# Kernel optimization log

Hardware: AMD Instinct MI355X
Metric: run time of the kernel (lower is better)

Reference implementation:

```python
import jax, jax.numpy as jnp
import numpy as np

B, S, E = 2, 2048, 1024
INNER = 2048          # proj_factor * embedding_dim
NH = 4                # mLSTM heads
K = 4                 # causal conv kernel size
PH, PD = 512, 4       # headwise-proj heads (inner/qkv_proj_blocksize) and block size


def setup_inputs() -> dict:
    key = jax.random.key(0)
    ks = jax.random.split(key, 10)
    f = lambda k, shape, s=0.02: jax.random.normal(k, shape, jnp.float32) * s
    return dict(
        x=jax.random.normal(ks[0], (B, S, E), jnp.float32),
        W_up=f(ks[1], (E, 2 * INNER)),
        conv_w=f(ks[2], (K, INNER), 0.1),
        conv_b=jnp.zeros((INNER,), jnp.float32),
        Wq=f(ks[3], (PH, PD, PD), 0.3),
        Wk=f(ks[4], (PH, PD, PD), 0.3),
        Wv=f(ks[5], (PH, PD, PD), 0.3),
        W_ig=f(ks[6], (3 * INNER, NH), 0.01),
        b_ig=jnp.zeros((NH,), jnp.float32),
        W_fg=f(ks[7], (3 * INNER, NH), 0.01),
        b_fg=jnp.linspace(3.0, 6.0, NH).astype(jnp.float32),
        norm_w=jnp.ones((INNER,), jnp.float32),
        skip=jnp.ones((INNER,), jnp.float32),
        W_down=f(ks[8], (INNER, E)),
    )


def _forward(x, W_up, conv_w, conv_b, Wq, Wk, Wv, W_ig, b_ig, W_fg, b_fg,
             norm_w, skip, W_down):
    Bx, Sx, _ = x.shape
    # up projection then split into mlstm branch and gate branch z
    x_inner = x @ W_up                                  # (B,S,2*INNER)
    x_mlstm, z = jnp.split(x_inner, 2, axis=-1)
    # causal depthwise conv1d (left-pad K-1)
    Kk = conv_w.shape[0]
    x_pad = jnp.pad(x_mlstm, ((0, 0), (Kk - 1, 0), (0, 0)))
    x_conv = sum(x_pad[:, i:i + Sx, :] * conv_w[i] for i in range(Kk)) + conv_b
    x_act = jax.nn.swish(x_conv)

    def headwise(t, W):
        H, o, d = W.shape
        return jnp.einsum('bshd,hod->bsho', t.reshape(Bx, Sx, H, d), W).reshape(Bx, Sx, H * o)

    q = headwise(x_act, Wq)
    k = headwise(x_act, Wk)
    v = headwise(x_mlstm, Wv)
    Dm = q.shape[-1]
    NHn = b_ig.shape[0]
    DH = Dm // NHn
    qh = q.reshape(Bx, Sx, NHn, DH).transpose(0, 2, 1, 3)   # (B,NH,S,DH)
    kh = k.reshape(Bx, Sx, NHn, DH).transpose(0, 2, 1, 3)
    vh = v.reshape(Bx, Sx, NHn, DH).transpose(0, 2, 1, 3)
    # input / forget gate preactivations from concat(q,k,v)
    if_in = jnp.concatenate([q, k, v], axis=-1)             # (B,S,3*INNER)
    ig = (if_in @ W_ig + b_ig).transpose(0, 2, 1)[..., None]  # (B,NH,S,1)
    fg = (if_in @ W_fg + b_fg).transpose(0, 2, 1)[..., None]
    # parallel stabilized mLSTM (matrix memory, exp gating)
    log_f = jax.nn.log_sigmoid(fg)
    lfc = jnp.concatenate([jnp.zeros((Bx, NHn, 1, 1), log_f.dtype),
                           jnp.cumsum(log_f, axis=2)], axis=2)  # (B,NH,S+1,1)
    lfm = lfc - jnp.swapaxes(lfc, -2, -1)                   # (B,NH,S+1,S+1)
    mask = jnp.tril(jnp.ones((Sx + 1, Sx + 1), bool))
    lfm = jnp.where(mask, lfm, -jnp.inf)[:, :, 1:, 1:]      # (B,NH,S,S)
    logD = lfm + jnp.swapaxes(ig, -2, -1)
    mD = jnp.max(logD, axis=-1, keepdims=True)
    Dmat = jnp.exp(logD - mD)
    C = jnp.einsum('bnsd,bntd->bnst', qh, kh) * (DH ** -0.5) * Dmat
    norm = jnp.maximum(jnp.abs(C.sum(-1, keepdims=True)), jnp.exp(-mD))
    h = jnp.einsum('bnst,bntd->bnsd', C / (norm + 1e-6), vh)  # (B,NH,S,DH)
    # multi-head layernorm over DH, then merge heads
    mu = h.mean(-1, keepdims=True)
    var = ((h - mu) ** 2).mean(-1, keepdims=True)
    hn = ((h - mu) * jax.lax.rsqrt(var + 1e-6)).transpose(0, 2, 1, 3).reshape(Bx, Sx, Dm)
    hn = hn * norm_w
    # learnable skip from conv activation, gate with swish(z), down proj
    h_state = (hn + skip * x_act) * jax.nn.swish(z)
    return h_state @ W_down


def reference(x, W_up, conv_w, conv_b, Wq, Wk, Wv, W_ig, b_ig, W_fg, b_fg,
              norm_w, skip, W_down):
    return _forward(x, W_up, conv_w, conv_b, Wq, Wk, Wv, W_ig, b_ig, W_fg,
                    b_fg, norm_w, skip, W_down)
```

## Files before the change

kernel.cpp:

```cpp
#include <hip/hip_runtime.h>
#include <math.h>

#define S_LEN 2048
#define INNERD 2048
#define NHEAD 4
#define DHEAD 512
#define BATCH 2
#define SCALE_QK 0.044194173824159216f

typedef __attribute__((ext_vector_type(8))) short short8v;
typedef __attribute__((ext_vector_type(4))) float f32x4;

#define MFMA_BF16(A, B, C) __builtin_amdgcn_mfma_f32_16x16x32_bf16(A, B, C, 0, 0, 0)

__device__ __forceinline__ void gll16(const void* g, void* l) {
  __builtin_amdgcn_global_load_lds((const __attribute__((address_space(1))) unsigned int*)g,
                                   (__attribute__((address_space(3))) unsigned int*)l,
                                   16, 0, 0);
}

__device__ __forceinline__ unsigned short f2bf(float x) {
  union { float f; unsigned u; } v; v.f = x;
  unsigned r = v.u + 0x7FFFu + ((v.u >> 16) & 1u);
  return (unsigned short)(r >> 16);
}
__device__ __forceinline__ float bf2f(unsigned short x) {
  union { unsigned u; float f; } v; v.u = ((unsigned)x) << 16; return v.f;
}
__device__ __forceinline__ float swishf(float x) { return x / (1.0f + __expf(-x)); }
__device__ __forceinline__ float logsigf(float x) {
  return (x >= 0.0f) ? -log1pf(expf(-x)) : (x - log1pf(expf(x)));
}

__global__ __launch_bounds__(256) void cast_kernel(const float* __restrict__ src,
                                                   unsigned short* __restrict__ dst) {
  const int i = (blockIdx.x * 256 + threadIdx.x) * 8;
  const float4 a = *(const float4*)(src + i);
  const float4 b = *(const float4*)(src + i + 4);
  short8v o;
  o[0] = (short)f2bf(a.x); o[1] = (short)f2bf(a.y); o[2] = (short)f2bf(a.z); o[3] = (short)f2bf(a.w);
  o[4] = (short)f2bf(b.x); o[5] = (short)f2bf(b.y); o[6] = (short)f2bf(b.z); o[7] = (short)f2bf(b.w);
  *(short8v*)(dst + i) = o;
}

__global__ __launch_bounds__(256) void trc_kernel(const float* __restrict__ src,
                                                  unsigned short* __restrict__ dst,
                                                  int R, int C) {
  const int t = threadIdx.x;
  const int r0 = blockIdx.y * 128, c0 = blockIdx.x * 128;
  const int rb = (t >> 4) * 8, cb2 = (t & 15) * 8;
  float vreg[8][8];
#pragma unroll
  for (int u = 0; u < 8; ++u) {
    const float4 p0 = *(const float4*)(src + (size_t)(r0 + rb + u) * C + c0 + cb2);
    const float4 p1 = *(const float4*)(src + (size_t)(r0 + rb + u) * C + c0 + cb2 + 4);
    vreg[u][0] = p0.x; vreg[u][1] = p0.y; vreg[u][2] = p0.z; vreg[u][3] = p0.w;
    vreg[u][4] = p1.x; vreg[u][5] = p1.y; vreg[u][6] = p1.z; vreg[u][7] = p1.w;
  }
#pragma unroll
  for (int j = 0; j < 8; ++j) {
    short8v o;
#pragma unroll
    for (int u = 0; u < 8; ++u) o[u] = (short)f2bf(vreg[u][j]);
    *(short8v*)(dst + (size_t)(c0 + cb2 + j) * R + r0 + rb) = o;
  }
}

__global__ __launch_bounds__(256) void trv_kernel(const unsigned short* __restrict__ v,
                                                  unsigned short* __restrict__ vt) {
  const int t = threadIdx.x;
  const int s0 = blockIdx.x * 128;
  const int d0 = blockIdx.y * 128;
  const int bn = blockIdx.z;
  const int b = bn >> 2, n = bn & 3;
  const int sb = (t >> 4) * 8, db = (t & 15) * 8;
  unsigned short r[8][8];
#pragma unroll
  for (int u = 0; u < 8; ++u) {
    const short8v x2 = *(const short8v*)(v + (size_t)(b * S_LEN + s0 + sb + u) * INNERD + n * DHEAD + d0 + db);
#pragma unroll
    for (int j = 0; j < 8; ++j) r[u][j] = (unsigned short)x2[j];
  }
#pragma unroll
  for (int j = 0; j < 8; ++j) {
    short8v o;
#pragma unroll
    for (int u = 0; u < 8; ++u) o[u] = (short)r[u][j];
    *(short8v*)(vt + (size_t)(bn * DHEAD + d0 + db + j) * S_LEN + s0 + sb) = o;
  }
}

__global__ __launch_bounds__(256) void prep_kernel(
    const float* __restrict__ Wq, const float* __restrict__ Wk, const float* __restrict__ Wv,
    const float* __restrict__ Wig, const float* __restrict__ Wfg,
    unsigned short* __restrict__ Wpk, unsigned short* __restrict__ CgT) {
  const int t = threadIdx.x;
  float wq[2][16], wk[2][16], wv[2][16];
#pragma unroll
  for (int hh = 0; hh < 2; ++hh) {
    const int h = 2 * t + hh;
#pragma unroll
    for (int j = 0; j < 16; ++j) {
      wq[hh][j] = Wq[(size_t)h * 16 + j];
      wk[hh][j] = Wk[(size_t)h * 16 + j];
      wv[hh][j] = Wv[(size_t)h * 16 + j];
    }
  }
#pragma unroll
  for (int hh = 0; hh < 2; ++hh)
#pragma unroll
    for (int sub = 0; sub < 2; ++sub) {
      short8v oq, ok, ov;
#pragma unroll
      for (int j = 0; j < 8; ++j) {
        oq[j] = (short)f2bf(wq[hh][sub * 8 + j]);
        ok[j] = (short)f2bf(wk[hh][sub * 8 + j]);
        ov[j] = (short)f2bf(wv[hh][sub * 8 + j]);
      }
      *(short8v*)(Wpk + ((size_t)(0 + hh * 2 + sub) * 256 + t) * 8) = oq;
      *(short8v*)(Wpk + ((size_t)(4 + hh * 2 + sub) * 256 + t) * 8) = ok;
      *(short8v*)(Wpk + ((size_t)(8 + hh * 2 + sub) * 256 + t) * 8) = ov;
    }
#pragma unroll
  for (int u = 0; u < 8; ++u) {
    const int hh = u >> 2, d = u & 3;
    const int h = 2 * t + hh;
    float cia[4] = {0, 0, 0, 0}, cim[4] = {0, 0, 0, 0};
    float cfa[4] = {0, 0, 0, 0}, cfm[4] = {0, 0, 0, 0};
#pragma unroll
    for (int o = 0; o < 4; ++o) {
      const int row = h * 4 + o;
      const float aq = wq[hh][o * 4 + d], ak = wk[hh][o * 4 + d], av = wv[hh][o * 4 + d];
#pragma unroll
      for (int g = 0; g < 4; ++g) {
        cia[g] += aq * Wig[(size_t)row * 4 + g] + ak * Wig[(size_t)(INNERD + row) * 4 + g];
        cim[g] += av * Wig[(size_t)(2 * INNERD + row) * 4 + g];
        cfa[g] += aq * Wfg[(size_t)row * 4 + g] + ak * Wfg[(size_t)(INNERD + row) * 4 + g];
        cfm[g] += av * Wfg[(size_t)(2 * INNERD + row) * 4 + g];
      }
    }
    const int c = t * 8 + u;
#pragma unroll
    for (int g = 0; g < 4; ++g) {
      CgT[(size_t)(g) * INNERD + c] = f2bf(cia[g]);
      CgT[(size_t)(4 + g) * INNERD + c] = f2bf(cim[g]);
      CgT[(size_t)(8 + g) * INNERD + c] = f2bf(cfa[g]);
      CgT[(size_t)(12 + g) * INNERD + c] = f2bf(cfm[g]);
    }
  }
}

template <int OUTMODE>
__global__ __launch_bounds__(256) void gemm_bf16(const unsigned short* __restrict__ A,
                                                 const unsigned short* __restrict__ Bt,
                                                 float* __restrict__ Cf,
                                                 unsigned short* __restrict__ Cb0,
                                                 unsigned short* __restrict__ Cb1,
                                                 int M, int N, int K) {
  __shared__ unsigned short As[128 * 64];
  __shared__ unsigned short Bs[128 * 64];
  const int tid = threadIdx.x;
  const int w = tid >> 6, l = tid & 63;
  const int lm = l & 15, l4 = l >> 4, l8 = l & 7, lr = l >> 3;
  const int nwg = gridDim.x * gridDim.y;
  int bid = blockIdx.y * gridDim.x + blockIdx.x;
  const int cpx = nwg >> 3;
  bid = (bid & 7) * cpx + (bid >> 3);
  const int bx = bid % gridDim.x, by = bid / gridDim.x;
  const int row0 = by * 128, col0 = bx * 128;
  const int wm = w >> 1, wn = w & 1;
  f32x4 acc[16];
#pragma unroll
  for (int i2 = 0; i2 < 16; ++i2) acc[i2] = (f32x4){0.f, 0.f, 0.f, 0.f};

  const int scol = (l8 * 16) ^ (lr << 4);

  for (int k0 = 0; k0 < K; k0 += 64) {
#pragma unroll
    for (int it = 0; it < 4; ++it) {
      const int r = it * 32 + w * 8 + lr;
      gll16((const char*)A + ((size_t)(row0 + r) * K + k0) * 2 + scol,
            (char*)As + (size_t)(it * 32 + w * 8) * 128);
      gll16((const char*)Bt + ((size_t)(col0 + r) * K + k0) * 2 + scol,
            (char*)Bs + (size_t)(it * 32 + w * 8) * 128);
    }
    __syncthreads();
#pragma unroll
    for (int ks = 0; ks < 2; ++ks) {
      short8v af[4], bfr[4];
#pragma unroll
      for (int rb = 0; rb < 4; ++rb) {
        const int row = wm * 64 + rb * 16 + lm;
        af[rb] = *(const short8v*)((const char*)As + row * 128 + ((ks * 64 + l4 * 16) ^ ((lm & 7) << 4)));
      }
#pragma unroll
      for (int cb = 0; cb < 4; ++cb) {
        const int row = wn * 64 + cb * 16 + lm;
        bfr[cb] = *(const short8v*)((const char*)Bs + row * 128 + ((ks * 64 + l4 * 16) ^ ((lm & 7) << 4)));
      }
      __builtin_amdgcn_s_setprio(1);
#pragma unroll
      for (int rb = 0; rb < 4; ++rb)
#pragma unroll
        for (int cb = 0; cb < 4; ++cb)
          acc[rb * 4 + cb] = MFMA_BF16(af[rb], bfr[cb], acc[rb * 4 + cb]);
      __builtin_amdgcn_s_setprio(0);
    }
    __syncthreads();
  }
#pragma unroll
  for (int rb = 0; rb < 4; ++rb)
#pragma unroll
    for (int cb = 0; cb < 4; ++cb)
#pragma unroll
      for (int r = 0; r < 4; ++r) {
        const int gr = row0 + wm * 64 + rb * 16 + l4 * 4 + r;
        const int gc = col0 + wn * 64 + cb * 16 + lm;
        const float vv = acc[rb * 4 + cb][r];
        if (OUTMODE == 0) {
          Cf[(size_t)gr * N + gc] = vv;
        } else {
          if (gc < 2048) Cb0[(size_t)gr * 2048 + gc] = f2bf(vv);
          else Cb1[(size_t)gr * 2048 + gc - 2048] = f2bf(vv);
        }
      }
}

__global__ __launch_bounds__(256) void headwise_kernel(
    const unsigned short* __restrict__ xm,
    const unsigned short* __restrict__ Wpk, const unsigned short* __restrict__ CgT,
    const float* __restrict__ cw, const float* __restrict__ cbias,
    const float* __restrict__ big, const float* __restrict__ bfg,
    unsigned short* __restrict__ q, unsigned short* __restrict__ k,
    unsigned short* __restrict__ v,
    float* __restrict__ igpre, float* __restrict__ fgpre) {
  __shared__ float red2[4][8];
  const int bs = blockIdx.x, t = threadIdx.x;
  const int s = bs & (S_LEN - 1);
  const int c0 = t * 8;
  float xa8[8], xm8[8];
  {
    float accv[8];
    const float4 cb0 = *(const float4*)(cbias + c0);
    const float4 cb1 = *(const float4*)(cbias + c0 + 4);
    accv[0] = cb0.x; accv[1] = cb0.y; accv[2] = cb0.z; accv[3] = cb0.w;
    accv[4] = cb1.x; accv[5] = cb1.y; accv[6] = cb1.z; accv[7] = cb1.w;
#pragma unroll
    for (int i = 0; i < 4; ++i) {
      if (s - 3 + i >= 0) {
        const short8v xv = *(const short8v*)(xm + (size_t)(bs - 3 + i) * INNERD + c0);
        const float4 w0 = *(const float4*)(cw + i * INNERD + c0);
        const float4 w1 = *(const float4*)(cw + i * INNERD + c0 + 4);
        const float wv2[8] = {w0.x, w0.y, w0.z, w0.w, w1.x, w1.y, w1.z, w1.w};
#pragma unroll
        for (int u = 0; u < 8; ++u) accv[u] += bf2f((unsigned short)xv[u]) * wv2[u];
      }
    }
    const short8v xs = *(const short8v*)(xm + (size_t)bs * INNERD + c0);
#pragma unroll
    for (int u = 0; u < 8; ++u) { xm8[u] = bf2f((unsigned short)xs[u]); xa8[u] = swishf(accv[u]); }
  }
  short8v qo, ko, vo;
#pragma unroll
  for (int hh = 0; hh < 2; ++hh)
#pragma unroll
    for (int sub = 0; sub < 2; ++sub) {
      const short8v wq = *(const short8v*)(Wpk + ((size_t)(0 + hh * 2 + sub) * 256 + t) * 8);
      const short8v wk = *(const short8v*)(Wpk + ((size_t)(4 + hh * 2 + sub) * 256 + t) * 8);
      const short8v wv3 = *(const short8v*)(Wpk + ((size_t)(8 + hh * 2 + sub) * 256 + t) * 8);
      float ql = 0, qh = 0, kl = 0, kh2 = 0, vl = 0, vh = 0;
#pragma unroll
      for (int d = 0; d < 4; ++d) {
        const float xa = xa8[hh * 4 + d], xv2 = xm8[hh * 4 + d];
        ql += bf2f((unsigned short)wq[d]) * xa;
        qh += bf2f((unsigned short)wq[4 + d]) * xa;
        kl += bf2f((unsigned short)wk[d]) * xa;
        kh2 += bf2f((unsigned short)wk[4 + d]) * xa;
        vl += bf2f((unsigned short)wv3[d]) * xv2;
        vh += bf2f((unsigned short)wv3[4 + d]) * xv2;
      }
      qo[hh * 4 + sub * 2] = (short)f2bf(ql); qo[hh * 4 + sub * 2 + 1] = (short)f2bf(qh);
      ko[hh * 4 + sub * 2] = (short)f2bf(kl); ko[hh * 4 + sub * 2 + 1] = (short)f2bf(kh2);
      vo[hh * 4 + sub * 2] = (short)f2bf(vl); vo[hh * 4 + sub * 2 + 1] = (short)f2bf(vh);
    }
  *(short8v*)(q + (size_t)bs * INNERD + c0) = qo;
  *(short8v*)(k + (size_t)bs * INNERD + c0) = ko;
  *(short8v*)(v + (size_t)bs * INNERD + c0) = vo;
  float r8[8];
#pragma unroll
  for (int j = 0; j < 4; ++j) {
    const short8v ca = *(const short8v*)(CgT + (size_t)j * INNERD + c0);
    const short8v cm = *(const short8v*)(CgT + (size_t)(4 + j) * INNERD + c0);
    const short8v fa = *(const short8v*)(CgT + (size_t)(8 + j) * INNERD + c0);
    const short8v fm = *(const short8v*)(CgT + (size_t)(12 + j) * INNERD + c0);
    float si = 0.f, sf = 0.f;
#pragma unroll
    for (int u = 0; u < 8; ++u) {
      si += xa8[u] * bf2f((unsigned short)ca[u]) + xm8[u] * bf2f((unsigned short)cm[u]);
      sf += xa8[u] * bf2f((unsigned short)fa[u]) + xm8[u] * bf2f((unsigned short)fm[u]);
    }
    r8[j] = si; r8[4 + j] = sf;
  }
  const int l = t & 63;
  const bool b1 = (l & 1), b2 = (l & 2), b4 = (l & 4);
  float t4[4];
#pragma unroll
  for (int i = 0; i < 4; ++i) {
    const float send = b1 ? r8[i] : r8[i + 4];
    const float recv = __shfl_xor(send, 1, 64);
    t4[i] = (b1 ? r8[i + 4] : r8[i]) + recv;
  }
  float u2[2];
#pragma unroll
  for (int i = 0; i < 2; ++i) {
    const float send = b2 ? t4[i] : t4[i + 2];
    const float recv = __shfl_xor(send, 2, 64);
    u2[i] = (b2 ? t4[i + 2] : t4[i]) + recv;
  }
  float wsum;
  {
    const float send = b4 ? u2[0] : u2[1];
    const float recv = __shfl_xor(send, 4, 64);
    wsum = (b4 ? u2[1] : u2[0]) + recv;
  }
  wsum += __shfl_xor(wsum, 8, 64);
  wsum += __shfl_xor(wsum, 16, 64);
  wsum += __shfl_xor(wsum, 32, 64);
  if (l < 8) {
    const int perm = ((l & 1) << 2) | (l & 2) | ((l >> 2) & 1);
    red2[t >> 6][perm] = wsum;
  }
  __syncthreads();
  if (t < 8) {
    const float sum = red2[0][t] + red2[1][t] + red2[2][t] + red2[3][t];
    const int b = bs >> 11;
    if (t < 4) igpre[((size_t)(b * NHEAD + t)) * S_LEN + s] = sum + big[t];
    else fgpre[((size_t)(b * NHEAD + t - 4)) * S_LEN + s] = sum + bfg[t - 4];
  }
}

__global__ __launch_bounds__(256) void scan_kernel(const float* __restrict__ igpre,
                                                   const float* __restrict__ fgpre,
                                                   float* __restrict__ a_o,
                                                   float* __restrict__ rm_o,
                                                   float* __restrict__ e_o) {
  __shared__ float sd[256];
  const int bn = blockIdx.x, t = threadIdx.x;
  const size_t base = (size_t)bn * S_LEN + t * 8;
  float cs[8];
  float run = 0.0f;
#pragma unroll
  for (int u = 0; u < 8; ++u) { run += logsigf(fgpre[base + u]); cs[u] = run; }
  sd[t] = run;
  __syncthreads();
  for (int off = 1; off < 256; off <<= 1) {
    const float vv2 = (t >= off) ? sd[t - off] : 0.0f;
    __syncthreads();
    sd[t] += vv2;
    __syncthreads();
  }
  const float exs = (t > 0) ? sd[t - 1] : 0.0f;
  __syncthreads();
  float av[8], pm[8];
  float rmax = -INFINITY;
#pragma unroll
  for (int u = 0; u < 8; ++u) {
    const float L = exs + cs[u];
    cs[u] = L;
    av[u] = igpre[base + u] - L;
    rmax = fmaxf(rmax, av[u]);
    pm[u] = rmax;
  }
  sd[t] = rmax;
  __syncthreads();
  for (int off = 1; off < 256; off <<= 1) {
    const float vv2 = (t >= off) ? sd[t - off] : -INFINITY;
    __syncthreads();
    sd[t] = fmaxf(sd[t], vv2);
    __syncthreads();
  }
  const float exm = (t > 0) ? sd[t - 1] : -INFINITY;
#pragma unroll
  for (int u = 0; u < 8; ++u) {
    const float rmv = fmaxf(exm, pm[u]);
    a_o[base + u] = av[u];
    rm_o[base + u] = rmv;
    e_o[base + u] = expf(-(cs[u] + rmv));
  }
}

__global__ __launch_bounds__(512) void mlstm_mfma(
    const unsigned short* __restrict__ qg, const unsigned short* __restrict__ kg,
    const unsigned short* __restrict__ vtg,
    const float* __restrict__ ag, const float* __restrict__ rmg,
    float* __restrict__ hraw, float* __restrict__ rsumg) {
  __shared__ unsigned short Ks[64 * 512];
  __shared__ unsigned short Ps[64 * 64];
  __shared__ float rsl[8][16];
  const int tid = threadIdx.x;
  const int w = tid >> 6, l = tid & 63;
  const int lm = l & 15, l4 = l >> 4;
  const int beta = blockIdx.x;
  const int bn = beta & 7;
  const int part = (beta >> 3) & 1;
  const int idx = beta >> 4;
  const int qi = (idx < 16) ? (31 - idx) : (idx - 16);
  const int i0 = qi << 6;
  const int b = bn >> 2, n = bn & 3;
  float* hp = hraw + (size_t)part * ((size_t)BATCH * S_LEN * INNERD);
  float* rp = rsumg + (size_t)part * ((size_t)BATCH * NHEAD * S_LEN);

  const int rA = ((w >> 1) << 4) + lm;
  short8v qf[16];
  {
    const unsigned short* qp = qg + (size_t)(b * S_LEN + i0 + rA) * INNERD + n * DHEAD + l4 * 8;
#pragma unroll
    for (int ks = 0; ks < 16; ++ks) qf[ks] = *(const short8v*)(qp + ks * 32);
  }
  const int rD = ((w >> 1) << 4) + (l4 << 2);
  float rm4[4];
#pragma unroll
  for (int r = 0; r < 4; ++r) rm4[r] = rmg[(size_t)bn * S_LEN + i0 + rD + r];
  const int cb0 = (w & 1) << 1;

  f32x4 acc[16];
#pragma unroll
  for (int i2 = 0; i2 < 16; ++i2) acc[i2] = (f32x4){0.f, 0.f, 0.f, 0.f};
  float rs4[4] = {0.f, 0.f, 0.f, 0.f};

  const int Tn = qi + 1;
  for (int jt = part; jt < Tn; jt += 2) {
    const int j0 = jt << 6;
    short8v vf[8];
#pragma unroll
    for (int db = 0; db < 4; ++db)
#pragma unroll
      for (int ks = 0; ks < 2; ++ks)
        vf[db * 2 + ks] = *(const short8v*)(vtg + (size_t)(bn * DHEAD + w * 64 + db * 16 + lm) * S_LEN + j0 + ks * 32 + l4 * 8);
    const float a0 = ag[(size_t)bn * S_LEN + j0 + cb0 * 16 + lm];
    const float a1 = ag[(size_t)bn * S_LEN + j0 + cb0 * 16 + 16 + lm];
#pragma unroll
    for (int it = 0; it < 8; ++it) {
      const int row = it * 8 + w;
      gll16((const char*)kg + ((size_t)(b * S_LEN + j0 + row) * INNERD + n * DHEAD) * 2 + ((l * 16) ^ ((row & 7) << 4)),
            (char*)Ks + row * 1024);
    }
    __syncthreads();
    f32x4 s0 = (f32x4){0.f, 0.f, 0.f, 0.f}, s1 = (f32x4){0.f, 0.f, 0.f, 0.f};
    __builtin_amdgcn_s_setprio(1);
#pragma unroll
    for (int ks = 0; ks < 16; ++ks) {
      const short8v b0 = *(const short8v*)((const char*)Ks + (cb0 * 16 + lm) * 1024 + ((ks * 64 + l4 * 16) ^ ((lm & 7) << 4)));
      const short8v b1 = *(const short8v*)((const char*)Ks + ((cb0 + 1) * 16 + lm) * 1024 + ((ks * 64 + l4 * 16) ^ ((lm & 7) << 4)));
      s0 = MFMA_BF16(qf[ks], b0, s0);
      s1 = MFMA_BF16(qf[ks], b1, s1);
    }
    __builtin_amdgcn_s_setprio(0);
#pragma unroll
    for (int half = 0; half < 2; ++half) {
      const f32x4 sv = half ? s1 : s0;
      const float av = half ? a1 : a0;
      const int jl = (cb0 + half) * 16 + lm;
#pragma unroll
      for (int r = 0; r < 4; ++r) {
        const int il = rD + r;
        const float es = __expf(av - rm4[r]);
        const float p = (j0 + jl <= i0 + il) ? sv[r] * SCALE_QK * es : 0.0f;
        rs4[r] += p;
        *((unsigned short*)((char*)Ps + il * 128 + ((jl * 2) ^ ((il & 7) << 4)))) = f2bf(p);
      }
    }
    __syncthreads();
#pragma unroll
    for (int ks = 0; ks < 2; ++ks) {
      short8v pa[4];
#pragma unroll
      for (int rb = 0; rb < 4; ++rb)
        pa[rb] = *(const short8v*)((const char*)Ps + (rb * 16 + lm) * 128 + ((ks * 64 + l4 * 16) ^ ((lm & 7) << 4)));
      __builtin_amdgcn_s_setprio(1);
#pragma unroll
      for (int rb = 0; rb < 4; ++rb)
#pragma unroll
        for (int db = 0; db < 4; ++db)
          acc[rb * 4 + db] = MFMA_BF16(pa[rb], vf[db * 2 + ks], acc[rb * 4 + db]);
      __builtin_amdgcn_s_setprio(0);
    }
    __syncthreads();
  }
#pragma unroll
  for (int r = 0; r < 4; ++r) {
    float v2 = rs4[r];
    v2 += __shfl_xor(v2, 1, 64);
    v2 += __shfl_xor(v2, 2, 64);
    v2 += __shfl_xor(v2, 4, 64);
    v2 += __shfl_xor(v2, 8, 64);
    if (lm == 0) rsl[w][l4 * 4 + r] = v2;
  }
  __syncthreads();
  if (tid < 64) {
    const int rblk = tid >> 4, rloc = tid & 15;
    rp[(size_t)bn * S_LEN + i0 + rblk * 16 + rloc] = rsl[rblk * 2][rloc] + rsl[rblk * 2 + 1][rloc];
  }
#pragma unroll
  for (int rb = 0; rb < 4; ++rb)
#pragma unroll
    for (int db = 0; db < 4; ++db) {
      float* dst = hp + (size_t)(b * S_LEN + i0 + rb * 16 + l4 * 4) * INNERD + n * DHEAD + w * 64 + db * 16 + lm;
#pragma unroll
      for (int r = 0; r < 4; ++r) dst[(size_t)r * INNERD] = acc[rb * 4 + db][r];
    }
}

__global__ __launch_bounds__(256) void mhln_kernel(
    const float* __restrict__ h, const unsigned short* __restrict__ xm,
    const unsigned short* __restrict__ zb,
    const float* __restrict__ cw, const float* __restrict__ cbias,
    const float* __restrict__ rsumg, const float* __restrict__ eg,
    const float* __restrict__ normw, const float* __restrict__ skip,
    unsigned short* __restrict__ hstate) {
  const int bs = blockIdx.x, t = threadIdx.x;
  const int bb = bs >> 11, s = bs & (S_LEN - 1);
  const int n = t >> 6, lane = t & 63;
  const int cp0 = n * DHEAD + lane * 8;
  const size_t hb = (size_t)bs * INNERD + cp0;
  const size_t HOFF = (size_t)BATCH * S_LEN * INNERD;
  const int bn = bb * NHEAD + n;
  const float rsv = rsumg[(size_t)bn * S_LEN + s] + rsumg[(size_t)BATCH * NHEAD * S_LEN + bn * S_LEN + s];
  const float ev = eg[(size_t)bn * S_LEN + s];
  const float inorm = 1.0f / (fmaxf(fabsf(rsv), ev) + 1e-6f);
  const float4 v0 = *(const float4*)(h + hb);
  const float4 v1 = *(const float4*)(h + hb + 4);
  const float4 u0 = *(const float4*)(h + HOFF + hb);
  const float4 u1 = *(const float4*)(h + HOFF + hb + 4);
  float vals[8] = {(v0.x + u0.x) * inorm, (v0.y + u0.y) * inorm, (v0.z + u0.z) * inorm,
                   (v0.w + u0.w) * inorm, (v1.x + u1.x) * inorm, (v1.y + u1.y) * inorm,
                   (v1.z + u1.z) * inorm, (v1.w + u1.w) * inorm};
  float sum = 0.0f;
#pragma unroll
  for (int u = 0; u < 8; ++u) sum += vals[u];
#pragma unroll
  for (int m = 32; m >= 1; m >>= 1) sum += __shfl_xor(sum, m, 64);
  const float mu = sum * (1.0f / 512.0f);
  float vs2 = 0.0f;
#pragma unroll
  for (int u = 0; u < 8; ++u) { const float d = vals[u] - mu; vs2 += d * d; }
#pragma unroll
  for (int m = 32; m >= 1; m >>= 1) vs2 += __shfl_xor(vs2, m, 64);
  const float rstd = rsqrtf(vs2 * (1.0f / 512.0f) + 1e-6f);
  float xa8[8];
  {
    float accv[8];
#pragma unroll
    for (int u = 0; u < 8; ++u) accv[u] = cbias[cp0 + u];
#pragma unroll
    for (int i2 = 0; i2 < 4; ++i2) {
      const int sj = s - 3 + i2;
      if (sj >= 0) {
        const short8v xv = *(const short8v*)(xm + (size_t)(bs - 3 + i2) * INNERD + cp0);
#pragma unroll
        for (int u = 0; u < 8; ++u)
          accv[u] += bf2f((unsigned short)xv[u]) * cw[i2 * INNERD + cp0 + u];
      }
    }
#pragma unroll
    for (int u = 0; u < 8; ++u) xa8[u] = swishf(accv[u]);
  }
  const short8v zv = *(const short8v*)(zb + (size_t)bs * INNERD + cp0);
  short8v o;
#pragma unroll
  for (int u = 0; u < 8; ++u) {
    const int cp = cp0 + u;
    const float hn = (vals[u] - mu) * rstd * normw[cp];
    const float z = bf2f((unsigned short)zv[u]);
    o[u] = (short)f2bf((hn + skip[cp] * xa8[u]) * swishf(z));
  }
  *(short8v*)(hstate + hb) = o;
}

extern "C" void kernel_launch(void* const* d_in, const int* in_sizes, int n_in,
                              void* d_out, int out_size, void* d_ws, size_t ws_size,
                              hipStream_t stream) {
  const float* x     = (const float*)d_in[0];
  const float* Wup   = (const float*)d_in[1];
  const float* cw    = (const float*)d_in[2];
  const float* cb    = (const float*)d_in[3];
  const float* Wq    = (const float*)d_in[4];
  const float* Wk    = (const float*)d_in[5];
  const float* Wv    = (const float*)d_in[6];
  const float* Wig   = (const float*)d_in[7];
  const float* big   = (const float*)d_in[8];
  const float* Wfg   = (const float*)d_in[9];
  const float* bfg   = (const float*)d_in[10];
  const float* normw = (const float*)d_in[11];
  const float* skip  = (const float*)d_in[12];
  const float* Wdown = (const float*)d_in[13];
  float* out = (float*)d_out;

  float* ws = (float*)d_ws;
  size_t off = 0;
  const size_t MR = (size_t)BATCH * S_LEN;
  const size_t GSZ = (size_t)BATCH * NHEAD * S_LEN;
  unsigned short* xm  = (unsigned short*)(ws + off); off += MR * INNERD / 2;
  unsigned short* zb  = (unsigned short*)(ws + off); off += MR * INNERD / 2;
  float* hraw         = ws + off;                    off += 2 * MR * INNERD;
  unsigned short* qb  = (unsigned short*)(ws + off); off += MR * INNERD / 2;
  unsigned short* kb  = (unsigned short*)(ws + off); off += MR * INNERD / 2;
  unsigned short* vt  = (unsigned short*)(ws + off); off += MR * INNERD / 2;
  float* igpre  = ws + off; off += GSZ;
  float* fgpre  = ws + off; off += GSZ;
  float* a_buf  = ws + off; off += GSZ;
  float* rm_buf = ws + off; off += GSZ;
  float* e_buf  = ws + off; off += GSZ;
  float* rsum   = ws + off; off += 2 * GSZ;
  unsigned short* Wpk = (unsigned short*)(ws + off); off += 12 * 256 * 8 / 2;
  unsigned short* CgT = (unsigned short*)(ws + off); off += 16 * (size_t)INNERD / 2;
  if (ws_size < off * sizeof(float)) return;

  unsigned short* vb     = (unsigned short*)hraw;
  unsigned short* x_bf   = (unsigned short*)(hraw + MR * INNERD);
  unsigned short* WupT   = vt;
  unsigned short* WdT    = kb;
  unsigned short* hstate = qb;

  prep_kernel<<<1, 256, 0, stream>>>(Wq, Wk, Wv, Wig, Wfg, Wpk, CgT);
  cast_kernel<<<2048, 256, 0, stream>>>(x, x_bf);
  trc_kernel<<<dim3(32, 8), 256, 0, stream>>>(Wup, WupT, 1024, 4096);
  gemm_bf16<1><<<dim3(32, 32), 256, 0, stream>>>(x_bf, WupT, nullptr, xm, zb, 4096, 4096, 1024);
  headwise_kernel<<<4096, 256, 0, stream>>>(xm, Wpk, CgT, cw, cb, big, bfg,
                                            qb, kb, vb, igpre, fgpre);
  trv_kernel<<<dim3(16, 4, 8), 256, 0, stream>>>(vb, vt);
  scan_kernel<<<8, 256, 0, stream>>>(igpre, fgpre, a_buf, rm_buf, e_buf);
  mlstm_mfma<<<512, 512, 0, stream>>>(qb, kb, vt, a_buf, rm_buf, hraw, rsum);
  trc_kernel<<<dim3(8, 16), 256, 0, stream>>>(Wdown, WdT, 2048, 1024);
  mhln_kernel<<<4096, 256, 0, stream>>>(hraw, xm, zb, cw, cb, rsum, e_buf, normw, skip, hstate);
  gemm_bf16<0><<<dim3(8, 32), 256, 0, stream>>>(hstate, WdT, out, nullptr, nullptr, 4096, 1024, 2048);
}
```

Measured before the change: 427.7 us.

## Double-buffer K tiles in mLSTM kernel and narrow down-projection GEMM tiles

The mLSTM attention kernel now double-buffers the K tile in shared memory. The next tile's global-to-LDS load is issued before computing on the current one, with explicit vmcnt waits and raw barriers replacing __syncthreads, so load latency overlaps the MFMA work. The down-projection GEMM gets a templated N tile of 64, doubling its grid to 512 workgroups for better CU occupancy. The doubled LDS footprint and the hand-set wait counts add a risk of occupancy loss and ordering bugs.

```diff
diff --git a/kernel.cpp b/kernel.cpp
--- a/kernel.cpp
+++ b/kernel.cpp
@@ -150,15 +150,16 @@
   }
 }
 
-template <int OUTMODE>
+template <int BN, int OUTMODE>
 __global__ __launch_bounds__(256) void gemm_bf16(const unsigned short* __restrict__ A,
                                                  const unsigned short* __restrict__ Bt,
                                                  float* __restrict__ Cf,
                                                  unsigned short* __restrict__ Cb0,
                                                  unsigned short* __restrict__ Cb1,
                                                  int M, int N, int K) {
+  constexpr int CB = BN / 32;
   __shared__ unsigned short As[128 * 64];
-  __shared__ unsigned short Bs[128 * 64];
+  __shared__ unsigned short Bs[BN * 64];
   const int tid = threadIdx.x;
   const int w = tid >> 6, l = tid & 63;
   const int lm = l & 15, l4 = l >> 4, l8 = l & 7, lr = l >> 3;
@@ -167,11 +168,11 @@
   const int cpx = nwg >> 3;
   bid = (bid & 7) * cpx + (bid >> 3);
   const int bx = bid % gridDim.x, by = bid / gridDim.x;
-  const int row0 = by * 128, col0 = bx * 128;
+  const int row0 = by * 128, col0 = bx * BN;
   const int wm = w >> 1, wn = w & 1;
-  f32x4 acc[16];
-#pragma unroll
-  for (int i2 = 0; i2 < 16; ++i2) acc[i2] = (f32x4){0.f, 0.f, 0.f, 0.f};
+  f32x4 acc[4 * CB];
+#pragma unroll
+  for (int i2 = 0; i2 < 4 * CB; ++i2) acc[i2] = (f32x4){0.f, 0.f, 0.f, 0.f};
 
   const int scol = (l8 * 16) ^ (lr << 4);
 
@@ -181,29 +182,33 @@
       const int r = it * 32 + w * 8 + lr;
       gll16((const char*)A + ((size_t)(row0 + r) * K + k0) * 2 + scol,
             (char*)As + (size_t)(it * 32 + w * 8) * 128);
+    }
+#pragma unroll
+    for (int it = 0; it < BN / 32; ++it) {
+      const int r = it * 32 + w * 8 + lr;
       gll16((const char*)Bt + ((size_t)(col0 + r) * K + k0) * 2 + scol,
             (char*)Bs + (size_t)(it * 32 + w * 8) * 128);
     }
     __syncthreads();
 #pragma unroll
     for (int ks = 0; ks < 2; ++ks) {
-      short8v af[4], bfr[4];
+      short8v af[4], bfr[CB];
 #pragma unroll
       for (int rb = 0; rb < 4; ++rb) {
         const int row = wm * 64 + rb * 16 + lm;
         af[rb] = *(const short8v*)((const char*)As + row * 128 + ((ks * 64 + l4 * 16) ^ ((lm & 7) << 4)));
       }
 #pragma unroll
-      for (int cb = 0; cb < 4; ++cb) {
-        const int row = wn * 64 + cb * 16 + lm;
+      for (int cb = 0; cb < CB; ++cb) {
+        const int row = wn * (BN / 2) + cb * 16 + lm;
         bfr[cb] = *(const short8v*)((const char*)Bs + row * 128 + ((ks * 64 + l4 * 16) ^ ((lm & 7) << 4)));
       }
       __builtin_amdgcn_s_setprio(1);
 #pragma unroll
       for (int rb = 0; rb < 4; ++rb)
 #pragma unroll
-        for (int cb = 0; cb < 4; ++cb)
-          acc[rb * 4 + cb] = MFMA_BF16(af[rb], bfr[cb], acc[rb * 4 + cb]);
+        for (int cb = 0; cb < CB; ++cb)
+          acc[rb * CB + cb] = MFMA_BF16(af[rb], bfr[cb], acc[rb * CB + cb]);
       __builtin_amdgcn_s_setprio(0);
     }
     __syncthreads();
@@ -211,12 +216,12 @@
 #pragma unroll
   for (int rb = 0; rb < 4; ++rb)
 #pragma unroll
-    for (int cb = 0; cb < 4; ++cb)
+    for (int cb = 0; cb < CB; ++cb)
 #pragma unroll
       for (int r = 0; r < 4; ++r) {
         const int gr = row0 + wm * 64 + rb * 16 + l4 * 4 + r;
-        const int gc = col0 + wn * 64 + cb * 16 + lm;
-        const float vv = acc[rb * 4 + cb][r];
+        const int gc = col0 + wn * (BN / 2) + cb * 16 + lm;
+        const float vv = acc[rb * CB + cb][r];
         if (OUTMODE == 0) {
           Cf[(size_t)gr * N + gc] = vv;
         } else {
@@ -389,12 +394,12 @@
   }
 }
 
-__global__ __launch_bounds__(512) void mlstm_mfma(
+__global__ __launch_bounds__(512, 2) void mlstm_mfma(
     const unsigned short* __restrict__ qg, const unsigned short* __restrict__ kg,
     const unsigned short* __restrict__ vtg,
     const float* __restrict__ ag, const float* __restrict__ rmg,
     float* __restrict__ hraw, float* __restrict__ rsumg) {
-  __shared__ unsigned short Ks[64 * 512];
+  __shared__ unsigned short Ks[2][64 * 512];
   __shared__ unsigned short Ps[64 * 64];
   __shared__ float rsl[8][16];
   const int tid = threadIdx.x;
@@ -428,9 +433,21 @@
   for (int i2 = 0; i2 < 16; ++i2) acc[i2] = (f32x4){0.f, 0.f, 0.f, 0.f};
   float rs4[4] = {0.f, 0.f, 0.f, 0.f};
 
-  const int Tn = qi + 1;
-  for (int jt = part; jt < Tn; jt += 2) {
-    const int j0 = jt << 6;
+  const int ntau = (qi + 2 - part) >> 1;
+  __builtin_amdgcn_sched_barrier(0);
+  if (ntau > 0) {
+#pragma unroll
+    for (int it = 0; it < 8; ++it) {
+      const int row = it * 8 + w;
+      gll16((const char*)kg + ((size_t)(b * S_LEN + part * 64 + row) * INNERD + n * DHEAD) * 2 + ((l * 16) ^ (w << 4)),
+            (char*)Ks[0] + row * 1024);
+    }
+  }
+  __builtin_amdgcn_sched_barrier(0);
+
+  for (int tau = 0; tau < ntau; ++tau) {
+    const int j0 = (part + 2 * tau) << 6;
+    const int cur = tau & 1;
     short8v vf[8];
 #pragma unroll
     for (int db = 0; db < 4; ++db)
@@ -439,19 +456,30 @@
         vf[db * 2 + ks] = *(const short8v*)(vtg + (size_t)(bn * DHEAD + w * 64 + db * 16 + lm) * S_LEN + j0 + ks * 32 + l4 * 8);
     const float a0 = ag[(size_t)bn * S_LEN + j0 + cb0 * 16 + lm];
     const float a1 = ag[(size_t)bn * S_LEN + j0 + cb0 * 16 + 16 + lm];
-#pragma unroll
-    for (int it = 0; it < 8; ++it) {
-      const int row = it * 8 + w;
-      gll16((const char*)kg + ((size_t)(b * S_LEN + j0 + row) * INNERD + n * DHEAD) * 2 + ((l * 16) ^ ((row & 7) << 4)),
-            (char*)Ks + row * 1024);
-    }
-    __syncthreads();
+    __builtin_amdgcn_sched_barrier(0);
+    const bool hasnext = (tau + 1 < ntau);
+    if (hasnext) {
+#pragma unroll
+      for (int it = 0; it < 8; ++it) {
+        const int row = it * 8 + w;
+        gll16((const char*)kg + ((size_t)(b * S_LEN + j0 + 128 + row) * INNERD + n * DHEAD) * 2 + ((l * 16) ^ (w << 4)),
+              (char*)Ks[cur ^ 1] + row * 1024);
+      }
+    }
+    __builtin_amdgcn_sched_barrier(0);
+    if (hasnext) { asm volatile("s_waitcnt vmcnt(18)" ::: "memory"); }
+    else         { asm volatile("s_waitcnt vmcnt(10)" ::: "memory"); }
+    __builtin_amdgcn_sched_barrier(0);
+    __builtin_amdgcn_s_barrier();
     f32x4 s0 = (f32x4){0.f, 0.f, 0.f, 0.f}, s1 = (f32x4){0.f, 0.f, 0.f, 0.f};
+    const char* kb0 = (const char*)Ks[cur] + (cb0 * 16 + lm) * 1024;
+    const char* kb1 = (const char*)Ks[cur] + ((cb0 + 1) * 16 + lm) * 1024;
     __builtin_amdgcn_s_setprio(1);
 #pragma unroll
     for (int ks = 0; ks < 16; ++ks) {
-      const short8v b0 = *(const short8v*)((const char*)Ks + (cb0 * 16 + lm) * 1024 + ((ks * 64 + l4 * 16) ^ ((lm & 7) << 4)));
-      const short8v b1 = *(const short8v*)((const char*)Ks + ((cb0 + 1) * 16 + lm) * 1024 + ((ks * 64 + l4 * 16) ^ ((lm & 7) << 4)));
+      const int off = (ks * 64 + l4 * 16) ^ ((lm & 7) << 4);
+      const short8v b0 = *(const short8v*)(kb0 + off);
+      const short8v b1 = *(const short8v*)(kb1 + off);
       s0 = MFMA_BF16(qf[ks], b0, s0);
       s1 = MFMA_BF16(qf[ks], b1, s1);
     }
@@ -470,7 +498,9 @@
         *((unsigned short*)((char*)Ps + il * 128 + ((jl * 2) ^ ((il & 7) << 4)))) = f2bf(p);
       }
     }
-    __syncthreads();
+    asm volatile("s_waitcnt lgkmcnt(0)" ::: "memory");
+    __builtin_amdgcn_sched_barrier(0);
+    __builtin_amdgcn_s_barrier();
 #pragma unroll
     for (int ks = 0; ks < 2; ++ks) {
       short8v pa[4];
@@ -485,7 +515,6 @@
           acc[rb * 4 + db] = MFMA_BF16(pa[rb], vf[db * 2 + ks], acc[rb * 4 + db]);
       __builtin_amdgcn_s_setprio(0);
     }
-    __syncthreads();
   }
 #pragma unroll
   for (int r = 0; r < 4; ++r) {
@@ -496,7 +525,8 @@
     v2 += __shfl_xor(v2, 8, 64);
     if (lm == 0) rsl[w][l4 * 4 + r] = v2;
   }
-  __syncthreads();
+  asm volatile("s_waitcnt lgkmcnt(0)" ::: "memory");
+  __builtin_amdgcn_s_barrier();
   if (tid < 64) {
     const int rblk = tid >> 4, rloc = tid & 15;
     rp[(size_t)bn * S_LEN + i0 + rblk * 16 + rloc] = rsl[rblk * 2][rloc] + rsl[rblk * 2 + 1][rloc];
@@ -625,7 +655,7 @@
   prep_kernel<<<1, 256, 0, stream>>>(Wq, Wk, Wv, Wig, Wfg, Wpk, CgT);
   cast_kernel<<<2048, 256, 0, stream>>>(x, x_bf);
   trc_kernel<<<dim3(32, 8), 256, 0, stream>>>(Wup, WupT, 1024, 4096);
-  gemm_bf16<1><<<dim3(32, 32), 256, 0, stream>>>(x_bf, WupT, nullptr, xm, zb, 4096, 4096, 1024);
+  gemm_bf16<128, 1><<<dim3(32, 32), 256, 0, stream>>>(x_bf, WupT, nullptr, xm, zb, 4096, 4096, 1024);
   headwise_kernel<<<4096, 256, 0, stream>>>(xm, Wpk, CgT, cw, cb, big, bfg,
                                             qb, kb, vb, igpre, fgpre);
   trv_kernel<<<dim3(16, 4, 8), 256, 0, stream>>>(vb, vt);
@@ -633,5 +663,5 @@
   mlstm_mfma<<<512, 512, 0, stream>>>(qb, kb, vt, a_buf, rm_buf, hraw, rsum);
   trc_kernel<<<dim3(8, 16), 256, 0, stream>>>(Wdown, WdT, 2048, 1024);
   mhln_kernel<<<4096, 256, 0, stream>>>(hraw, xm, zb, cw, cb, rsum, e_buf, normw, skip, hstate);
-  gemm_bf16<0><<<dim3(8, 32), 256, 0, stream>>>(hstate, WdT, out, nullptr, nullptr, 4096, 1024, 2048);
-}
+  gemm_bf16<64, 0><<<dim3(16, 32), 256, 0, stream>>>(hstate, WdT, out, nullptr, nullptr, 4096, 1024, 2048);
+}
```

Result: faster. 396.2 us (-7.4%).
